# Kernel tuning notes

Measured on AMD Instinct MI355X. Metric: run time of the kernel, lower is better.

## Reference

```python
import jax, jax.numpy as jnp
import numpy as np

B, N, D = 16, 1024, 768
NEG = -1.0e9

def leaky_relu(x, slope=0.01):
    return jnp.where(x >= 0, x, slope * x)

def setup_inputs() -> dict:
    key = jax.random.key(0)
    ks = jax.random.split(key, 20)
    s = 0.02
    inp = {
        'inputs': jax.random.normal(ks[0], (B, N, D), dtype=jnp.float32),
        'adj_mat': jax.random.randint(ks[1], (B, N, N), 0, 2).astype(jnp.float32),
        # BaseGraphAttNet params
        'W_fc': jax.random.normal(ks[2], (D, D), dtype=jnp.float32) * s,
        'b_fc': jnp.zeros((D,), dtype=jnp.float32),
        'w_q': jax.random.normal(ks[3], (D,), dtype=jnp.float32) * s,
        'b_q': jnp.zeros((), dtype=jnp.float32),
        'w_k': jax.random.normal(ks[4], (D,), dtype=jnp.float32) * s,
        'b_k': jnp.zeros((), dtype=jnp.float32),
        # gating params (6 linears)
        'W_uy': jax.random.normal(ks[5], (D, D), dtype=jnp.float32) * s,
        'b_uy': jnp.zeros((D,), dtype=jnp.float32),
        'W_ux': jax.random.normal(ks[6], (D, D), dtype=jnp.float32) * s,
        'b_ux': jnp.zeros((D,), dtype=jnp.float32),
        'W_ry': jax.random.normal(ks[7], (D, D), dtype=jnp.float32) * s,
        'b_ry': jnp.zeros((D,), dtype=jnp.float32),
        'W_rx': jax.random.normal(ks[8], (D, D), dtype=jnp.float32) * s,
        'b_rx': jnp.zeros((D,), dtype=jnp.float32),
        'W_ty': jax.random.normal(ks[9], (D, D), dtype=jnp.float32) * s,
        'b_ty': jnp.zeros((D,), dtype=jnp.float32),
        'W_tx': jax.random.normal(ks[10], (D, D), dtype=jnp.float32) * s,
        'b_tx': jnp.zeros((D,), dtype=jnp.float32),
    }
    return inp

def reference(inputs, adj_mat, W_fc, b_fc, w_q, b_q, w_k, b_k,
              W_uy, b_uy, W_ux, b_ux, W_ry, b_ry, W_rx, b_rx,
              W_ty, b_ty, W_tx, b_tx):
    # ---- BaseGraphAttNet (residual=False); dropout in eval mode (identity) ----
    feat_proj = jnp.einsum('bnd,ed->bne', inputs, W_fc) + b_fc      # bs x N x D
    q = jnp.einsum('bnd,d->bn', feat_proj, w_q) + b_q               # bs x N
    k = jnp.einsum('bnd,d->bn', feat_proj, w_k) + b_k               # bs x N
    logits = q[:, :, None] + k[:, None, :]                          # bs x N x N
    masked = logits + (1.0 - adj_mat) * NEG
    masked = leaky_relu(masked)
    att = jax.nn.softmax(masked, axis=-1)
    y = jnp.einsum('bnm,bmd->bnd', att, feat_proj)                  # bs x N x D
    # ---- GRU-style gating ----
    u = jax.nn.sigmoid(jnp.einsum('bnd,ed->bne', y, W_uy) + b_uy
                       + jnp.einsum('bnd,ed->bne', inputs, W_ux) + b_ux)
    r = jax.nn.sigmoid(jnp.einsum('bnd,ed->bne', y, W_ry) + b_ry
                       + jnp.einsum('bnd,ed->bne', inputs, W_rx) + b_rx)
    x_tmp = jnp.tanh(jnp.einsum('bnd,ed->bne', y, W_ty) + b_ty
                     + jnp.einsum('bnd,ed->bne', r * inputs, W_tx) + b_tx)
    out = (1.0 - u) * inputs + u * x_tmp
    return out
```

## Files before the change

### kernel.cpp

```cpp
#include <hip/hip_runtime.h>
#include <cmath>

typedef __attribute__((ext_vector_type(8))) short bf16x8;
typedef __attribute__((ext_vector_type(4))) float f32x4;
typedef unsigned short u16;

struct __align__(8) us4 { u16 x, y, z, w; };

__device__ __forceinline__ u16 f2bf(float f) {
    union { float f; unsigned u; } v; v.f = f;
    unsigned u = v.u;
    u += 0x7fffu + ((u >> 16) & 1u);
    return (u16)(u >> 16);
}
__device__ __forceinline__ float bf2f(u16 h) {
    union { unsigned u; float f; } v; v.u = ((unsigned)h) << 16;
    return v.f;
}
__device__ __forceinline__ f32x4 mfma16(bf16x8 a, bf16x8 b, f32x4 c) {
    return __builtin_amdgcn_mfma_f32_16x16x32_bf16(a, b, c, 0, 0, 0);
}
__device__ __forceinline__ void ld_lds16(const u16* g, u16* l) {
    __builtin_amdgcn_global_load_lds(
        (const __attribute__((address_space(1))) unsigned int*)g,
        (__attribute__((address_space(3))) unsigned int*)l, 16, 0, 0);
}

__global__ __launch_bounds__(256) void cvtx(const float* __restrict__ in,
                                            u16* __restrict__ CatA, float* __restrict__ qkz) {
    int i = blockIdx.x * 256 + threadIdx.x;
    float4 f = reinterpret_cast<const float4*>(in)[i];
    us4 o; o.x = f2bf(f.x); o.y = f2bf(f.y); o.z = f2bf(f.z); o.w = f2bf(f.w);
    int row = i / 192, col = (i % 192) * 4;
    *reinterpret_cast<us4*>(CatA + (size_t)row * 1536 + 768 + col) = o;
    if (i < 8192) reinterpret_cast<float4*>(qkz)[i] = float4{0.f, 0.f, 0.f, 0.f};
}

struct WCvt { const float* s[7]; u16* d[7]; int ld[7]; };
__global__ __launch_bounds__(256) void cvtw(WCvt w) {
    int wi = blockIdx.y;
    int i = blockIdx.x * 256 + threadIdx.x;
    float4 f = reinterpret_cast<const float4*>(w.s[wi])[i];
    us4 o; o.x = f2bf(f.x); o.y = f2bf(f.y); o.z = f2bf(f.z); o.w = f2bf(f.w);
    int row = i / 192, col = (i % 192) * 4;
    *reinterpret_cast<us4*>(w.d[wi] + (size_t)row * w.ld[wi] + col) = o;
}

enum { EPI_FPT = 0, EPI_Y, EPI_GATES, EPI_OUT };

struct Epi {
    const float* b1; const float* b2; const float* b3; const float* b4;
    const float* wq; const float* wk; float* qv; float* kv;
    u16* fpT;
    u16* catA;
    const u16* xb;
    u16* ub_o; u16* rxb_o;
    const u16* ub; float* of;
};

template<int EPI, int PH>
__global__ __launch_bounds__(256) void g128(
    const u16* __restrict__ A1, const u16* __restrict__ B1,
    const u16* __restrict__ A2, const u16* __restrict__ B2,
    int K, int ldA1, int ldB1, int ldA2, int ldB2,
    size_t zA, size_t zB, Epi e)
{
    __shared__ u16 lA[128 * 64];
    __shared__ u16 lB[128 * 64];

    const int t = threadIdx.x;
    const int w = t >> 6, lane = t & 63, lm = lane & 15, quad = lane >> 4;
    const int row0 = blockIdx.x * 128;
    int col0, grp = 0;
    if constexpr (EPI == EPI_GATES) { grp = blockIdx.y / 6; col0 = (blockIdx.y % 6) * 128; }
    else col0 = blockIdx.y * 128;

    const int rs2 = t >> 3;
    const int kc2 = (((t & 7) ^ (rs2 & 7)) * 8);
    u16* dA_[4]; u16* dB_[4];
#pragma unroll
    for (int q = 0; q < 4; q++) {
        dA_[q] = lA + q * 2048 + w * 512;
        dB_[q] = lB + q * 2048 + w * 512;
    }

    const int rw0 = (w & 1) * 64, cw0 = (w >> 1) * 64;
    const int ch0 = ((quad) ^ (lm & 7)) * 8;
    const int ch1 = ((quad + 4) ^ (lm & 7)) * 8;
    int laB[4], lbB[4];
#pragma unroll
    for (int i = 0; i < 4; i++) laB[i] = (rw0 + i * 16 + lm) * 64;
#pragma unroll
    for (int j = 0; j < 4; j++) lbB[j] = (cw0 + j * 16 + lm) * 64;

    f32x4 acc[4][4] = {};
    bool first = true;

#pragma unroll
    for (int ph = 0; ph < PH; ph++) {
        const u16* As; const u16* Bs; int ldA, ldB;
        if (ph == 0) { As = A1 + (size_t)blockIdx.z * zA; Bs = B1 + (size_t)blockIdx.z * zB; ldA = ldA1; ldB = ldB1; }
        else         { As = A2; Bs = B2; ldA = ldA2; ldB = ldB2; }
        if constexpr (EPI == EPI_GATES) Bs += (size_t)grp * (768 * 1536);
        const u16* gA = As + (size_t)(row0 + rs2) * ldA + kc2;
        const u16* gB = Bs + (size_t)(col0 + rs2) * ldB + kc2;

        for (int k0 = 0; k0 < K; k0 += 64) {
            if (!first) __syncthreads();
            first = false;
#pragma unroll
            for (int q = 0; q < 4; q++) {
                ld_lds16(gA + (size_t)(q * 32) * ldA + k0, dA_[q]);
                ld_lds16(gB + (size_t)(q * 32) * ldB + k0, dB_[q]);
            }
            __syncthreads();

#pragma unroll
            for (int h = 0; h < 2; h++) {
                const int ch = h ? ch1 : ch0;
                bf16x8 a[4], b[4];
#pragma unroll
                for (int i = 0; i < 4; i++) a[i] = *reinterpret_cast<const bf16x8*>(lA + laB[i] + ch);
#pragma unroll
                for (int j = 0; j < 4; j++) b[j] = *reinterpret_cast<const bf16x8*>(lB + lbB[j] + ch);
#pragma unroll
                for (int i = 0; i < 4; i++)
#pragma unroll
                    for (int j = 0; j < 4; j++)
                        acc[i][j] = mfma16(a[i], b[j], acc[i][j]);
            }
        }
    }

#pragma unroll
    for (int i = 0; i < 4; i++) {
        const int gr = row0 + rw0 + i * 16 + quad * 4;
        if constexpr (EPI == EPI_FPT) {
            float qp[4] = {}, kp[4] = {};
            int bb = gr >> 10, nn = gr & 1023;
#pragma unroll
            for (int j = 0; j < 4; j++) {
                int gc = col0 + cw0 + j * 16 + lm;
                float bias = e.b1[gc];
                float v0 = acc[i][j][0] + bias, v1 = acc[i][j][1] + bias;
                float v2 = acc[i][j][2] + bias, v3 = acc[i][j][3] + bias;
                us4 o; o.x = f2bf(v0); o.y = f2bf(v1); o.z = f2bf(v2); o.w = f2bf(v3);
                *reinterpret_cast<us4*>(e.fpT + (size_t)bb * 786432 + (size_t)gc * 1024 + nn) = o;
                float wqv = e.wq[gc], wkv = e.wk[gc];
                qp[0] = fmaf(v0, wqv, qp[0]); qp[1] = fmaf(v1, wqv, qp[1]);
                qp[2] = fmaf(v2, wqv, qp[2]); qp[3] = fmaf(v3, wqv, qp[3]);
                kp[0] = fmaf(v0, wkv, kp[0]); kp[1] = fmaf(v1, wkv, kp[1]);
                kp[2] = fmaf(v2, wkv, kp[2]); kp[3] = fmaf(v3, wkv, kp[3]);
            }
#pragma unroll
            for (int r = 0; r < 4; r++) {
                float q = qp[r], k = kp[r];
#pragma unroll
                for (int m = 1; m < 16; m <<= 1) { q += __shfl_xor(q, m); k += __shfl_xor(k, m); }
                if (lm == 0) { atomicAdd(e.qv + gr + r, q); atomicAdd(e.kv + gr + r, k); }
            }
        } else if constexpr (EPI == EPI_Y) {
            size_t grow = (size_t)blockIdx.z * 1024 + gr;
#pragma unroll
            for (int j = 0; j < 4; j++) {
                int gc = col0 + cw0 + j * 16 + lm;
#pragma unroll
                for (int r = 0; r < 4; r++)
                    e.catA[(grow + r) * 1536 + gc] = f2bf(acc[i][j][r]);
            }
        } else if constexpr (EPI == EPI_GATES) {
#pragma unroll
            for (int j = 0; j < 4; j++) {
                int gc = col0 + cw0 + j * 16 + lm;
                if (grp == 0) {
                    float bias = e.b1[gc] + e.b2[gc];
#pragma unroll
                    for (int r = 0; r < 4; r++) {
                        size_t idx = (size_t)(gr + r) * 768 + gc;
                        e.ub_o[idx] = f2bf(1.f / (1.f + __expf(-(acc[i][j][r] + bias))));
                    }
                } else {
                    float bias = e.b3[gc] + e.b4[gc];
#pragma unroll
                    for (int r = 0; r < 4; r++) {
                        size_t idx = (size_t)(gr + r) * 768 + gc;
                        float rr = 1.f / (1.f + __expf(-(acc[i][j][r] + bias)));
                        float xv = bf2f(e.xb[(size_t)(gr + r) * 1536 + gc]);
                        e.rxb_o[idx] = f2bf(rr * xv);
                    }
                }
            }
        } else {
#pragma unroll
            for (int j = 0; j < 4; j++) {
                int gc = col0 + cw0 + j * 16 + lm;
                float bias = e.b1[gc] + e.b2[gc];
#pragma unroll
                for (int r = 0; r < 4; r++) {
                    size_t idx = (size_t)(gr + r) * 768 + gc;
                    float tt = tanhf(acc[i][j][r] + bias);
                    float uu = bf2f(e.ub[idx]);
                    float xv = bf2f(e.xb[(size_t)(gr + r) * 1536 + gc]);
                    e.of[idx] = (1.f - uu) * xv + uu * tt;
                }
            }
        }
    }
}

__global__ __launch_bounds__(256) void k_soft4(const float* __restrict__ adj,
                                               const float* __restrict__ qv,
                                               const float* __restrict__ kv,
                                               const float* __restrict__ bq,
                                               const float* __restrict__ bk,
                                               u16* __restrict__ attb) {
    int wv = threadIdx.x >> 6, lane = threadIdx.x & 63;
    int bn = blockIdx.x * 4 + wv;
    int b = bn >> 10;
    const float* adjrow = adj + (size_t)bn * 1024 + lane * 16;
    const float* krow = kv + (b << 10) + lane * 16;
    float q = qv[bn] + bq[0] + bk[0];

    float v[16];
#pragma unroll
    for (int c = 0; c < 4; c++) {
        float4 a4 = *reinterpret_cast<const float4*>(adjrow + c * 4);
        float4 k4 = *reinterpret_cast<const float4*>(krow + c * 4);
        float* vv = v + c * 4;
        vv[0] = q + k4.x + (1.f - a4.x) * -1.0e9f;
        vv[1] = q + k4.y + (1.f - a4.y) * -1.0e9f;
        vv[2] = q + k4.z + (1.f - a4.z) * -1.0e9f;
        vv[3] = q + k4.w + (1.f - a4.w) * -1.0e9f;
    }
#pragma unroll
    for (int t = 0; t < 16; t++) v[t] = v[t] >= 0.f ? v[t] : 0.01f * v[t];

    float mx = v[0];
#pragma unroll
    for (int t = 1; t < 16; t++) mx = fmaxf(mx, v[t]);
#pragma unroll
    for (int off = 32; off; off >>= 1) mx = fmaxf(mx, __shfl_xor(mx, off));

    float s = 0.f;
#pragma unroll
    for (int t = 0; t < 16; t++) { v[t] = __expf(v[t] - mx); s += v[t]; }
#pragma unroll
    for (int off = 32; off; off >>= 1) s += __shfl_xor(s, off);
    float inv = 1.f / s;

    u16* orow = attb + (size_t)bn * 1024 + lane * 16;
#pragma unroll
    for (int c = 0; c < 4; c++) {
        us4 o;
        o.x = f2bf(v[c * 4 + 0] * inv); o.y = f2bf(v[c * 4 + 1] * inv);
        o.z = f2bf(v[c * 4 + 2] * inv); o.w = f2bf(v[c * 4 + 3] * inv);
        *reinterpret_cast<us4*>(orow + c * 4) = o;
    }
}

extern "C" void kernel_launch(void* const* d_in, const int* in_sizes, int n_in,
                              void* d_out, int out_size, void* d_ws, size_t ws_size,
                              hipStream_t stream) {
    const float* x    = (const float*)d_in[0];
    const float* adj  = (const float*)d_in[1];
    const float* W_fc = (const float*)d_in[2];
    const float* b_fc = (const float*)d_in[3];
    const float* w_q  = (const float*)d_in[4];
    const float* b_q  = (const float*)d_in[5];
    const float* w_k  = (const float*)d_in[6];
    const float* b_k  = (const float*)d_in[7];
    const float* W_uy = (const float*)d_in[8];
    const float* b_uy = (const float*)d_in[9];
    const float* W_ux = (const float*)d_in[10];
    const float* b_ux = (const float*)d_in[11];
    const float* W_ry = (const float*)d_in[12];
    const float* b_ry = (const float*)d_in[13];
    const float* W_rx = (const float*)d_in[14];
    const float* b_rx = (const float*)d_in[15];
    const float* W_ty = (const float*)d_in[16];
    const float* b_ty = (const float*)d_in[17];
    const float* W_tx = (const float*)d_in[18];
    const float* b_tx = (const float*)d_in[19];

    char* ws = (char*)d_ws;
    u16*   CatA  = (u16*)  (ws + 0);
    u16*   Wfc_b = (u16*)  (ws + 50331648);
    u16*   Wty_b = (u16*)  (ws + 51511296);
    u16*   Wtx_b = (u16*)  (ws + 52690944);
    u16*   Wg    = (u16*)  (ws + 53870592);
    u16*   fpT   = (u16*)  (ws + 58589184);
    float* qv    = (float*)(ws + 83755008);
    float* kv    = (float*)(ws + 83820544);
    u16*   attb  = (u16*)  (ws + 83886080);
    u16*   u_b   = (u16*)  (ws + 83886080);
    u16*   rxb   = (u16*)  (ws + 117440512);

    cvtx<<<12288, 256, 0, stream>>>(x, CatA, qv);

    WCvt wc;
    wc.s[0] = W_fc; wc.d[0] = Wfc_b;              wc.ld[0] = 768;
    wc.s[1] = W_ty; wc.d[1] = Wty_b;              wc.ld[1] = 768;
    wc.s[2] = W_tx; wc.d[2] = Wtx_b;              wc.ld[2] = 768;
    wc.s[3] = W_uy; wc.d[3] = Wg;                 wc.ld[3] = 1536;
    wc.s[4] = W_ux; wc.d[4] = Wg + 768;           wc.ld[4] = 1536;
    wc.s[5] = W_ry; wc.d[5] = Wg + 768 * 1536;    wc.ld[5] = 1536;
    wc.s[6] = W_rx; wc.d[6] = Wg + 768 * 1536 + 768; wc.ld[6] = 1536;
    cvtw<<<dim3(576, 7), 256, 0, stream>>>(wc);

    Epi e{};
    e = Epi{}; e.b1 = b_fc; e.wq = w_q; e.wk = w_k; e.qv = qv; e.kv = kv; e.fpT = fpT;
    g128<EPI_FPT, 1><<<dim3(128, 6), 256, 0, stream>>>(CatA + 768, Wfc_b, nullptr, nullptr,
                                                       768, 1536, 768, 0, 0, 0, 0, e);

    k_soft4<<<4096, 256, 0, stream>>>(adj, qv, kv, b_q, b_k, attb);

    e = Epi{}; e.catA = CatA;
    g128<EPI_Y, 1><<<dim3(8, 6, 16), 256, 0, stream>>>(attb, fpT, nullptr, nullptr,
                                                       1024, 1024, 1024, 0, 0,
                                                       1048576, 786432, e);
    e = Epi{}; e.b1 = b_uy; e.b2 = b_ux; e.b3 = b_ry; e.b4 = b_rx;
    e.xb = CatA + 768; e.ub_o = u_b; e.rxb_o = rxb;
    g128<EPI_GATES, 1><<<dim3(128, 12), 256, 0, stream>>>(CatA, Wg, nullptr, nullptr,
                                                          1536, 1536, 1536, 0, 0, 0, 0, e);
    e = Epi{}; e.b1 = b_ty; e.b2 = b_tx; e.ub = u_b; e.xb = CatA + 768; e.of = (float*)d_out;
    g128<EPI_OUT, 2><<<dim3(128, 6), 256, 0, stream>>>(CatA, Wty_b, rxb, Wtx_b,
                                                       768, 1536, 768, 768, 768, 0, 0, e);
}
```

Before: 438.2 us.

## Replace 128x128 GEMM with 256x192 tiles and a 4-stage async LDS pipeline

```diff
diff --git a/kernel.cpp b/kernel.cpp
--- a/kernel.cpp
+++ b/kernel.cpp
@@ -25,6 +25,8 @@
         (const __attribute__((address_space(1))) unsigned int*)g,
         (__attribute__((address_space(3))) unsigned int*)l, 16, 0, 0);
 }
+
+#define VMCNT(n) asm volatile("s_waitcnt vmcnt(" #n ")" ::: "memory")
 
 __global__ __launch_bounds__(256) void cvtx(const float* __restrict__ in,
                                             u16* __restrict__ CatA, float* __restrict__ qkz) {
@@ -58,95 +60,115 @@
     const u16* ub; float* of;
 };
 
-template<int EPI, int PH>
-__global__ __launch_bounds__(256) void g128(
+template<int EPI>
+__global__ __launch_bounds__(512, 2) void g256(
     const u16* __restrict__ A1, const u16* __restrict__ B1,
     const u16* __restrict__ A2, const u16* __restrict__ B2,
-    int K, int ldA1, int ldB1, int ldA2, int ldB2,
+    int nt1, int nt2, int ldA1, int ldB1, int ldA2, int ldB2,
     size_t zA, size_t zB, Epi e)
 {
-    __shared__ u16 lA[128 * 64];
-    __shared__ u16 lB[128 * 64];
+    __shared__ __align__(16) u16 lA[4 * 8192];
+    __shared__ __align__(16) u16 lB[4 * 6144];
 
     const int t = threadIdx.x;
     const int w = t >> 6, lane = t & 63, lm = lane & 15, quad = lane >> 4;
-    const int row0 = blockIdx.x * 128;
+    const int wm = w >> 1, wn = w & 1;
+    const int row0 = blockIdx.x * 256;
     int col0, grp = 0;
-    if constexpr (EPI == EPI_GATES) { grp = blockIdx.y / 6; col0 = (blockIdx.y % 6) * 128; }
-    else col0 = blockIdx.y * 128;
-
-    const int rs2 = t >> 3;
-    const int kc2 = (((t & 7) ^ (rs2 & 7)) * 8);
-    u16* dA_[4]; u16* dB_[4];
-#pragma unroll
-    for (int q = 0; q < 4; q++) {
-        dA_[q] = lA + q * 2048 + w * 512;
-        dB_[q] = lB + q * 2048 + w * 512;
+    if constexpr (EPI == EPI_GATES) { grp = blockIdx.y >> 2; col0 = (blockIdx.y & 3) * 192; }
+    else col0 = blockIdx.y * 192;
+
+    const u16* A1p = A1 + (size_t)blockIdx.z * zA;
+    const u16* B1p = B1 + (size_t)blockIdx.z * zB;
+    if constexpr (EPI == EPI_GATES) B1p += (size_t)grp * (768 * 1536);
+
+    const int NT = nt1 + nt2;
+
+    const int sr  = t >> 2;
+    const int sg  = ((t & 3) ^ ((sr >> 1) & 3)) * 8;
+    const int srd = (t & 255) >> 2;
+    const int sgd = ((t & 3) ^ ((srd >> 1) & 3)) * 8;
+
+    auto stageA = [&](int ti) {
+        const u16* S; int ld_, k0;
+        if (ti < nt1) { S = A1p; ld_ = ldA1; k0 = ti * 32; }
+        else          { S = A2;  ld_ = ldA2; k0 = (ti - nt1) * 32; }
+        const u16* s0 = S + (size_t)(row0 + sr) * ld_ + k0 + sg;
+        u16* d = lA + (ti & 3) * 8192 + w * 512;
+        ld_lds16(s0, d);
+        ld_lds16(s0 + (size_t)128 * ld_, d + 4096);
+    };
+    auto stageB = [&](int ti) {
+        const u16* S; int ld_, k0;
+        if (ti < nt1) { S = B1p; ld_ = ldB1; k0 = ti * 32; }
+        else          { S = B2;  ld_ = ldB2; k0 = (ti - nt1) * 32; }
+        const u16* s0 = S + (size_t)(col0 + sr) * ld_ + k0 + sg;
+        u16* d = lB + (ti & 3) * 6144 + w * 512;
+        ld_lds16(s0, d);
+        const u16* s1 = S + (size_t)(col0 + 128 + srd) * ld_ + k0 + sgd;
+        ld_lds16(s1, lB + (ti & 3) * 6144 + 4096 + (w & 3) * 512);
+    };
+
+    const int swz  = (quad ^ ((lm >> 1) & 3)) * 8;
+    const int aoff = (wm * 64 + lm) * 32 + swz;
+    const int boff = (wn * 96 + lm) * 32 + swz;
+
+    f32x4 acc[4][6] = {};
+
+    stageA(0); stageB(0); stageA(1); stageB(1);
+    VMCNT(4);
+    __builtin_amdgcn_s_barrier();
+
+    for (int tt = 0; tt < NT; ++tt) {
+        const u16* bufA = lA + (tt & 3) * 8192;
+        const u16* bufB = lB + (tt & 3) * 6144;
+        const bool pf = (tt + 2) < NT;
+
+        if (pf) stageA(tt + 2);
+        bf16x8 a[4], b[3];
+#pragma unroll
+        for (int i = 0; i < 4; i++) a[i] = *reinterpret_cast<const bf16x8*>(bufA + aoff + i * 512);
+#pragma unroll
+        for (int j = 0; j < 3; j++) b[j] = *reinterpret_cast<const bf16x8*>(bufB + boff + j * 512);
+        __builtin_amdgcn_s_setprio(1);
+#pragma unroll
+        for (int i = 0; i < 4; i++)
+#pragma unroll
+            for (int j = 0; j < 3; j++)
+                acc[i][j] = mfma16(a[i], b[j], acc[i][j]);
+        __builtin_amdgcn_s_setprio(0);
+        __builtin_amdgcn_s_barrier();
+
+        if (pf) stageB(tt + 2);
+#pragma unroll
+        for (int j = 0; j < 3; j++) b[j] = *reinterpret_cast<const bf16x8*>(bufB + boff + (j + 3) * 512);
+        __builtin_amdgcn_s_setprio(1);
+#pragma unroll
+        for (int i = 0; i < 4; i++)
+#pragma unroll
+            for (int j = 0; j < 3; j++)
+                acc[i][j + 3] = mfma16(a[i], b[j], acc[i][j + 3]);
+        __builtin_amdgcn_s_setprio(0);
+        if (pf) { VMCNT(4); } else { VMCNT(0); }
+        __builtin_amdgcn_s_barrier();
     }
 
-    const int rw0 = (w & 1) * 64, cw0 = (w >> 1) * 64;
-    const int ch0 = ((quad) ^ (lm & 7)) * 8;
-    const int ch1 = ((quad + 4) ^ (lm & 7)) * 8;
-    int laB[4], lbB[4];
-#pragma unroll
-    for (int i = 0; i < 4; i++) laB[i] = (rw0 + i * 16 + lm) * 64;
-#pragma unroll
-    for (int j = 0; j < 4; j++) lbB[j] = (cw0 + j * 16 + lm) * 64;
-
-    f32x4 acc[4][4] = {};
-    bool first = true;
-
-#pragma unroll
-    for (int ph = 0; ph < PH; ph++) {
-        const u16* As; const u16* Bs; int ldA, ldB;
-        if (ph == 0) { As = A1 + (size_t)blockIdx.z * zA; Bs = B1 + (size_t)blockIdx.z * zB; ldA = ldA1; ldB = ldB1; }
-        else         { As = A2; Bs = B2; ldA = ldA2; ldB = ldB2; }
-        if constexpr (EPI == EPI_GATES) Bs += (size_t)grp * (768 * 1536);
-        const u16* gA = As + (size_t)(row0 + rs2) * ldA + kc2;
-        const u16* gB = Bs + (size_t)(col0 + rs2) * ldB + kc2;
-
-        for (int k0 = 0; k0 < K; k0 += 64) {
-            if (!first) __syncthreads();
-            first = false;
-#pragma unroll
-            for (int q = 0; q < 4; q++) {
-                ld_lds16(gA + (size_t)(q * 32) * ldA + k0, dA_[q]);
-                ld_lds16(gB + (size_t)(q * 32) * ldB + k0, dB_[q]);
-            }
-            __syncthreads();
-
-#pragma unroll
-            for (int h = 0; h < 2; h++) {
-                const int ch = h ? ch1 : ch0;
-                bf16x8 a[4], b[4];
-#pragma unroll
-                for (int i = 0; i < 4; i++) a[i] = *reinterpret_cast<const bf16x8*>(lA + laB[i] + ch);
-#pragma unroll
-                for (int j = 0; j < 4; j++) b[j] = *reinterpret_cast<const bf16x8*>(lB + lbB[j] + ch);
-#pragma unroll
-                for (int i = 0; i < 4; i++)
-#pragma unroll
-                    for (int j = 0; j < 4; j++)
-                        acc[i][j] = mfma16(a[i], b[j], acc[i][j]);
-            }
-        }
-    }
-
+    const int rw0 = wm * 64, cw0 = wn * 96;
 #pragma unroll
     for (int i = 0; i < 4; i++) {
         const int gr = row0 + rw0 + i * 16 + quad * 4;
         if constexpr (EPI == EPI_FPT) {
             float qp[4] = {}, kp[4] = {};
-            int bb = gr >> 10, nn = gr & 1023;
-#pragma unroll
-            for (int j = 0; j < 4; j++) {
-                int gc = col0 + cw0 + j * 16 + lm;
-                float bias = e.b1[gc];
+            const int bb = gr >> 10, nn = gr & 1023;
+#pragma unroll
+            for (int j = 0; j < 6; j++) {
+                const int gc = col0 + cw0 + j * 16 + lm;
+                const float bias = e.b1[gc];
                 float v0 = acc[i][j][0] + bias, v1 = acc[i][j][1] + bias;
                 float v2 = acc[i][j][2] + bias, v3 = acc[i][j][3] + bias;
                 us4 o; o.x = f2bf(v0); o.y = f2bf(v1); o.z = f2bf(v2); o.w = f2bf(v3);
                 *reinterpret_cast<us4*>(e.fpT + (size_t)bb * 786432 + (size_t)gc * 1024 + nn) = o;
-                float wqv = e.wq[gc], wkv = e.wk[gc];
+                const float wqv = e.wq[gc], wkv = e.wk[gc];
                 qp[0] = fmaf(v0, wqv, qp[0]); qp[1] = fmaf(v1, wqv, qp[1]);
                 qp[2] = fmaf(v2, wqv, qp[2]); qp[3] = fmaf(v3, wqv, qp[3]);
                 kp[0] = fmaf(v0, wkv, kp[0]); kp[1] = fmaf(v1, wkv, kp[1]);
@@ -160,30 +182,30 @@
                 if (lm == 0) { atomicAdd(e.qv + gr + r, q); atomicAdd(e.kv + gr + r, k); }
             }
         } else if constexpr (EPI == EPI_Y) {
-            size_t grow = (size_t)blockIdx.z * 1024 + gr;
-#pragma unroll
-            for (int j = 0; j < 4; j++) {
-                int gc = col0 + cw0 + j * 16 + lm;
+            const size_t grow = (size_t)blockIdx.z * 1024 + gr;
+#pragma unroll
+            for (int j = 0; j < 6; j++) {
+                const int gc = col0 + cw0 + j * 16 + lm;
 #pragma unroll
                 for (int r = 0; r < 4; r++)
                     e.catA[(grow + r) * 1536 + gc] = f2bf(acc[i][j][r]);
             }
         } else if constexpr (EPI == EPI_GATES) {
 #pragma unroll
-            for (int j = 0; j < 4; j++) {
-                int gc = col0 + cw0 + j * 16 + lm;
+            for (int j = 0; j < 6; j++) {
+                const int gc = col0 + cw0 + j * 16 + lm;
                 if (grp == 0) {
-                    float bias = e.b1[gc] + e.b2[gc];
+                    const float bias = e.b1[gc] + e.b2[gc];
 #pragma unroll
                     for (int r = 0; r < 4; r++) {
-                        size_t idx = (size_t)(gr + r) * 768 + gc;
+                        const size_t idx = (size_t)(gr + r) * 768 + gc;
                         e.ub_o[idx] = f2bf(1.f / (1.f + __expf(-(acc[i][j][r] + bias))));
                     }
                 } else {
-                    float bias = e.b3[gc] + e.b4[gc];
+                    const float bias = e.b3[gc] + e.b4[gc];
 #pragma unroll
                     for (int r = 0; r < 4; r++) {
-                        size_t idx = (size_t)(gr + r) * 768 + gc;
+                        const size_t idx = (size_t)(gr + r) * 768 + gc;
                         float rr = 1.f / (1.f + __expf(-(acc[i][j][r] + bias)));
                         float xv = bf2f(e.xb[(size_t)(gr + r) * 1536 + gc]);
                         e.rxb_o[idx] = f2bf(rr * xv);
@@ -192,16 +214,16 @@
             }
         } else {
 #pragma unroll
-            for (int j = 0; j < 4; j++) {
-                int gc = col0 + cw0 + j * 16 + lm;
-                float bias = e.b1[gc] + e.b2[gc];
+            for (int j = 0; j < 6; j++) {
+                const int gc = col0 + cw0 + j * 16 + lm;
+                const float bias = e.b1[gc] + e.b2[gc];
 #pragma unroll
                 for (int r = 0; r < 4; r++) {
-                    size_t idx = (size_t)(gr + r) * 768 + gc;
-                    float tt = tanhf(acc[i][j][r] + bias);
+                    const size_t idx = (size_t)(gr + r) * 768 + gc;
+                    float tv = tanhf(acc[i][j][r] + bias);
                     float uu = bf2f(e.ub[idx]);
                     float xv = bf2f(e.xb[(size_t)(gr + r) * 1536 + gc]);
-                    e.of[idx] = (1.f - uu) * xv + uu * tt;
+                    e.of[idx] = (1.f - uu) * xv + uu * tv;
                 }
             }
         }
@@ -233,17 +255,17 @@
         vv[3] = q + k4.w + (1.f - a4.w) * -1.0e9f;
     }
 #pragma unroll
-    for (int t = 0; t < 16; t++) v[t] = v[t] >= 0.f ? v[t] : 0.01f * v[t];
+    for (int tt = 0; tt < 16; tt++) v[tt] = v[tt] >= 0.f ? v[tt] : 0.01f * v[tt];
 
     float mx = v[0];
 #pragma unroll
-    for (int t = 1; t < 16; t++) mx = fmaxf(mx, v[t]);
+    for (int tt = 1; tt < 16; tt++) mx = fmaxf(mx, v[tt]);
 #pragma unroll
     for (int off = 32; off; off >>= 1) mx = fmaxf(mx, __shfl_xor(mx, off));
 
     float s = 0.f;
 #pragma unroll
-    for (int t = 0; t < 16; t++) { v[t] = __expf(v[t] - mx); s += v[t]; }
+    for (int tt = 0; tt < 16; tt++) { v[tt] = __expf(v[tt] - mx); s += v[tt]; }
 #pragma unroll
     for (int off = 32; off; off >>= 1) s += __shfl_xor(s, off);
     float inv = 1.f / s;
@@ -309,20 +331,20 @@
 
     Epi e{};
     e = Epi{}; e.b1 = b_fc; e.wq = w_q; e.wk = w_k; e.qv = qv; e.kv = kv; e.fpT = fpT;
-    g128<EPI_FPT, 1><<<dim3(128, 6), 256, 0, stream>>>(CatA + 768, Wfc_b, nullptr, nullptr,
-                                                       768, 1536, 768, 0, 0, 0, 0, e);
+    g256<EPI_FPT><<<dim3(64, 4), 512, 0, stream>>>(CatA + 768, Wfc_b, nullptr, nullptr,
+                                                   24, 0, 1536, 768, 0, 0, 0, 0, e);
 
     k_soft4<<<4096, 256, 0, stream>>>(adj, qv, kv, b_q, b_k, attb);
 
     e = Epi{}; e.catA = CatA;
-    g128<EPI_Y, 1><<<dim3(8, 6, 16), 256, 0, stream>>>(attb, fpT, nullptr, nullptr,
-                                                       1024, 1024, 1024, 0, 0,
-                                                       1048576, 786432, e);
+    g256<EPI_Y><<<dim3(4, 4, 16), 512, 0, stream>>>(attb, fpT, nullptr, nullptr,
+                                                    32, 0, 1024, 1024, 0, 0,
+                                                    1048576, 786432, e);
     e = Epi{}; e.b1 = b_uy; e.b2 = b_ux; e.b3 = b_ry; e.b4 = b_rx;
     e.xb = CatA + 768; e.ub_o = u_b; e.rxb_o = rxb;
-    g128<EPI_GATES, 1><<<dim3(128, 12), 256, 0, stream>>>(CatA, Wg, nullptr, nullptr,
-                                                          1536, 1536, 1536, 0, 0, 0, 0, e);
+    g256<EPI_GATES><<<dim3(64, 8), 512, 0, stream>>>(CatA, Wg, nullptr, nullptr,
+                                                     48, 0, 1536, 1536, 0, 0, 0, 0, e);
     e = Epi{}; e.b1 = b_ty; e.b2 = b_tx; e.ub = u_b; e.xb = CatA + 768; e.of = (float*)d_out;
-    g128<EPI_OUT, 2><<<dim3(128, 6), 256, 0, stream>>>(CatA, Wty_b, rxb, Wtx_b,
-                                                       768, 1536, 768, 768, 768, 0, 0, e);
-}
+    g256<EPI_OUT><<<dim3(64, 4), 512, 0, stream>>>(CatA, Wty_b, rxb, Wtx_b,
+                                                   24, 24, 1536, 768, 768, 768, 0, 0, e);
+}
```

After: 554.3 us. 1.26x slower.

## Triple-buffer LDS tiles with async prefetch in the bf16 GEMM kernel

Applied to the files above, without the earlier changes.

```diff
diff --git a/kernel.cpp b/kernel.cpp
--- a/kernel.cpp
+++ b/kernel.cpp
@@ -25,6 +25,8 @@
         (const __attribute__((address_space(1))) unsigned int*)g,
         (__attribute__((address_space(3))) unsigned int*)l, 16, 0, 0);
 }
+
+#define VMCNT(n) asm volatile("s_waitcnt vmcnt(" #n ")" ::: "memory")
 
 __global__ __launch_bounds__(256) void cvtx(const float* __restrict__ in,
                                             u16* __restrict__ CatA, float* __restrict__ qkz) {
@@ -58,15 +60,15 @@
     const u16* ub; float* of;
 };
 
-template<int EPI, int PH>
+template<int EPI>
 __global__ __launch_bounds__(256) void g128(
     const u16* __restrict__ A1, const u16* __restrict__ B1,
     const u16* __restrict__ A2, const u16* __restrict__ B2,
-    int K, int ldA1, int ldB1, int ldA2, int ldB2,
+    int nt1, int nt2, int ldA1, int ldB1, int ldA2, int ldB2,
     size_t zA, size_t zB, Epi e)
 {
-    __shared__ u16 lA[128 * 64];
-    __shared__ u16 lB[128 * 64];
+    __shared__ __align__(16) u16 lA[3 * 4096];
+    __shared__ __align__(16) u16 lB[3 * 4096];
 
     const int t = threadIdx.x;
     const int w = t >> 6, lane = t & 63, lm = lane & 15, quad = lane >> 4;
@@ -75,61 +77,70 @@
     if constexpr (EPI == EPI_GATES) { grp = blockIdx.y / 6; col0 = (blockIdx.y % 6) * 128; }
     else col0 = blockIdx.y * 128;
 
-    const int rs2 = t >> 3;
-    const int kc2 = (((t & 7) ^ (rs2 & 7)) * 8);
-    u16* dA_[4]; u16* dB_[4];
-#pragma unroll
-    for (int q = 0; q < 4; q++) {
-        dA_[q] = lA + q * 2048 + w * 512;
-        dB_[q] = lB + q * 2048 + w * 512;
-    }
+    const u16* A1p = A1 + (size_t)blockIdx.z * zA;
+    const u16* B1p = B1 + (size_t)blockIdx.z * zB;
+    if constexpr (EPI == EPI_GATES) B1p += (size_t)grp * (768 * 1536);
+    const int NT = nt1 + nt2;
+
+    const int sr = t >> 2;
+    const int sc = ((t & 3) ^ ((sr >> 1) & 3)) * 8;
+
+    auto stage = [&](int ti, int bi) {
+        const u16 *Sa, *Sb; int lda_, ldb_, k0;
+        if (ti < nt1) { Sa = A1p; Sb = B1p; lda_ = ldA1; ldb_ = ldB1; k0 = ti * 32; }
+        else          { Sa = A2;  Sb = B2;  lda_ = ldA2; ldb_ = ldB2; k0 = (ti - nt1) * 32; }
+        u16* dA = lA + bi * 4096 + w * 512;
+        u16* dB = lB + bi * 4096 + w * 512;
+        const u16* ga = Sa + (size_t)(row0 + sr) * lda_ + k0 + sc;
+        const u16* gb = Sb + (size_t)(col0 + sr) * ldb_ + k0 + sc;
+        ld_lds16(ga, dA);
+        ld_lds16(ga + (size_t)64 * lda_, dA + 2048);
+        ld_lds16(gb, dB);
+        ld_lds16(gb + (size_t)64 * ldb_, dB + 2048);
+    };
 
     const int rw0 = (w & 1) * 64, cw0 = (w >> 1) * 64;
-    const int ch0 = ((quad) ^ (lm & 7)) * 8;
-    const int ch1 = ((quad + 4) ^ (lm & 7)) * 8;
+    const int swz = (quad ^ ((lm >> 1) & 3)) * 8;
     int laB[4], lbB[4];
 #pragma unroll
-    for (int i = 0; i < 4; i++) laB[i] = (rw0 + i * 16 + lm) * 64;
-#pragma unroll
-    for (int j = 0; j < 4; j++) lbB[j] = (cw0 + j * 16 + lm) * 64;
+    for (int i = 0; i < 4; i++) laB[i] = (rw0 + i * 16 + lm) * 32 + swz;
+#pragma unroll
+    for (int j = 0; j < 4; j++) lbB[j] = (cw0 + j * 16 + lm) * 32 + swz;
 
     f32x4 acc[4][4] = {};
-    bool first = true;
-
-#pragma unroll
-    for (int ph = 0; ph < PH; ph++) {
-        const u16* As; const u16* Bs; int ldA, ldB;
-        if (ph == 0) { As = A1 + (size_t)blockIdx.z * zA; Bs = B1 + (size_t)blockIdx.z * zB; ldA = ldA1; ldB = ldB1; }
-        else         { As = A2; Bs = B2; ldA = ldA2; ldB = ldB2; }
-        if constexpr (EPI == EPI_GATES) Bs += (size_t)grp * (768 * 1536);
-        const u16* gA = As + (size_t)(row0 + rs2) * ldA + kc2;
-        const u16* gB = Bs + (size_t)(col0 + rs2) * ldB + kc2;
-
-        for (int k0 = 0; k0 < K; k0 += 64) {
-            if (!first) __syncthreads();
-            first = false;
-#pragma unroll
-            for (int q = 0; q < 4; q++) {
-                ld_lds16(gA + (size_t)(q * 32) * ldA + k0, dA_[q]);
-                ld_lds16(gB + (size_t)(q * 32) * ldB + k0, dB_[q]);
-            }
-            __syncthreads();
-
-#pragma unroll
-            for (int h = 0; h < 2; h++) {
-                const int ch = h ? ch1 : ch0;
-                bf16x8 a[4], b[4];
-#pragma unroll
-                for (int i = 0; i < 4; i++) a[i] = *reinterpret_cast<const bf16x8*>(lA + laB[i] + ch);
-#pragma unroll
-                for (int j = 0; j < 4; j++) b[j] = *reinterpret_cast<const bf16x8*>(lB + lbB[j] + ch);
-#pragma unroll
-                for (int i = 0; i < 4; i++)
-#pragma unroll
-                    for (int j = 0; j < 4; j++)
-                        acc[i][j] = mfma16(a[i], b[j], acc[i][j]);
-            }
+
+    stage(0, 0); stage(1, 1);
+    VMCNT(4);
+    __builtin_amdgcn_s_barrier();
+    __builtin_amdgcn_sched_barrier(0);
+
+    int bcur = 0, bpre = 2;
+    for (int tt = 0; tt < NT; ++tt) {
+        if (tt + 2 < NT) stage(tt + 2, bpre);
+
+        const u16* bA = lA + bcur * 4096;
+        const u16* bB = lB + bcur * 4096;
+        bf16x8 a[4], b[4];
+#pragma unroll
+        for (int i = 0; i < 4; i++) a[i] = *reinterpret_cast<const bf16x8*>(bA + laB[i]);
+#pragma unroll
+        for (int j = 0; j < 4; j++) b[j] = *reinterpret_cast<const bf16x8*>(bB + lbB[j]);
+
+        __builtin_amdgcn_s_setprio(1);
+#pragma unroll
+        for (int i = 0; i < 4; i++)
+#pragma unroll
+            for (int j = 0; j < 4; j++)
+                acc[i][j] = mfma16(a[i], b[j], acc[i][j]);
+        __builtin_amdgcn_s_setprio(0);
+
+        if (tt + 1 < NT) {
+            if (tt + 2 < NT) { VMCNT(4); } else { VMCNT(0); }
+            __builtin_amdgcn_s_barrier();
+            __builtin_amdgcn_sched_barrier(0);
         }
+        bcur = (bcur == 2) ? 0 : bcur + 1;
+        bpre = (bpre == 2) ? 0 : bpre + 1;
     }
 
 #pragma unroll
@@ -309,20 +320,20 @@
 
     Epi e{};
     e = Epi{}; e.b1 = b_fc; e.wq = w_q; e.wk = w_k; e.qv = qv; e.kv = kv; e.fpT = fpT;
-    g128<EPI_FPT, 1><<<dim3(128, 6), 256, 0, stream>>>(CatA + 768, Wfc_b, nullptr, nullptr,
-                                                       768, 1536, 768, 0, 0, 0, 0, e);
+    g128<EPI_FPT><<<dim3(128, 6), 256, 0, stream>>>(CatA + 768, Wfc_b, nullptr, nullptr,
+                                                    24, 0, 1536, 768, 0, 0, 0, 0, e);
 
     k_soft4<<<4096, 256, 0, stream>>>(adj, qv, kv, b_q, b_k, attb);
 
     e = Epi{}; e.catA = CatA;
-    g128<EPI_Y, 1><<<dim3(8, 6, 16), 256, 0, stream>>>(attb, fpT, nullptr, nullptr,
-                                                       1024, 1024, 1024, 0, 0,
-                                                       1048576, 786432, e);
+    g128<EPI_Y><<<dim3(8, 6, 16), 256, 0, stream>>>(attb, fpT, nullptr, nullptr,
+                                                    32, 0, 1024, 1024, 0, 0,
+                                                    1048576, 786432, e);
     e = Epi{}; e.b1 = b_uy; e.b2 = b_ux; e.b3 = b_ry; e.b4 = b_rx;
     e.xb = CatA + 768; e.ub_o = u_b; e.rxb_o = rxb;
-    g128<EPI_GATES, 1><<<dim3(128, 12), 256, 0, stream>>>(CatA, Wg, nullptr, nullptr,
-                                                          1536, 1536, 1536, 0, 0, 0, 0, e);
+    g128<EPI_GATES><<<dim3(128, 12), 256, 0, stream>>>(CatA, Wg, nullptr, nullptr,
+                                                       48, 0, 1536, 1536, 0, 0, 0, 0, e);
     e = Epi{}; e.b1 = b_ty; e.b2 = b_tx; e.ub = u_b; e.xb = CatA + 768; e.of = (float*)d_out;
-    g128<EPI_OUT, 2><<<dim3(128, 6), 256, 0, stream>>>(CatA, Wty_b, rxb, Wtx_b,
-                                                       768, 1536, 768, 768, 768, 0, 0, e);
-}
+    g128<EPI_OUT><<<dim3(128, 6), 256, 0, stream>>>(CatA, Wty_b, rxb, Wtx_b,
+                                                    24, 24, 1536, 768, 768, 768, 0, 0, e);
+}
```

After: 477.1 us. 1.09x slower.
